# Kernel optimization log

Hardware: AMD Instinct MI355X
Metric: run time of the kernel (lower is better)

Reference implementation:

```python
import jax, jax.numpy as jnp
import numpy as np

D_MODEL = 1024
N_HEADS = 16
HEAD_DIM = D_MODEL // N_HEADS
ROPE_BASE = 10000.0


def setup_inputs() -> dict:
    key = jax.random.key(0)
    ks = jax.random.split(key, 5)
    B, S = 4, 2048
    bound_qkv = 1.0 / np.sqrt(D_MODEL)
    bound_out = 1.0 / np.sqrt(D_MODEL)
    return {
        "query": jax.random.normal(ks[0], (B, S, D_MODEL), dtype=jnp.float32),
        "W_qkv": jax.random.uniform(ks[1], (3 * D_MODEL, D_MODEL), jnp.float32, -bound_qkv, bound_qkv),
        "b_qkv": jax.random.uniform(ks[2], (3 * D_MODEL,), jnp.float32, -bound_qkv, bound_qkv),
        "W_out": jax.random.uniform(ks[3], (D_MODEL, D_MODEL), jnp.float32, -bound_out, bound_out),
        "b_out": jax.random.uniform(ks[4], (D_MODEL,), jnp.float32, -bound_out, bound_out),
    }


def _rope(x):
    # x: [B, H, S, Dh]; rotate-half RoPE, full rotational fraction
    S, Dh = x.shape[2], x.shape[3]
    half = Dh // 2
    inv_freq = 1.0 / (ROPE_BASE ** (jnp.arange(0, half, dtype=jnp.float32) * 2.0 / Dh))
    ang = jnp.arange(S, dtype=jnp.float32)[:, None] * inv_freq[None, :]  # [S, half]
    cos = jnp.concatenate([jnp.cos(ang), jnp.cos(ang)], axis=-1)  # [S, Dh]
    sin = jnp.concatenate([jnp.sin(ang), jnp.sin(ang)], axis=-1)
    x1, x2 = x[..., :half], x[..., half:]
    rot = jnp.concatenate([-x2, x1], axis=-1)
    return x * cos + rot * sin


def reference(query, W_qkv, b_qkv, W_out, b_out):
    B, S, _ = query.shape
    qkv = query @ W_qkv.T + b_qkv  # [B, S, 3*D]
    qkv = qkv.reshape(B, S, 3, N_HEADS, HEAD_DIM).transpose(2, 0, 3, 1, 4)  # [3, B, H, S, Dh]
    q, k, v = qkv[0], qkv[1], qkv[2]
    q = _rope(q)
    k = _rope(k)
    scale = 1.0 / np.sqrt(HEAD_DIM)
    scores = jnp.einsum("bhsd,bhtd->bhst", q, k) * scale  # [B, H, S, S]
    attn = jax.nn.softmax(scores, axis=-1)
    out = jnp.einsum("bhst,bhtd->bhsd", attn, v)  # [B, H, S, Dh]
    out = out.transpose(0, 2, 1, 3).reshape(B, S, D_MODEL)
    return out @ W_out.T + b_out
```

## Files before the change

### kernel.cpp

```cpp
#include <hip/hip_runtime.h>
#include <math.h>

#define D_MODEL 1024
#define N_HEADS 16
#define HEAD_DIM 64
#define BATCH 4
#define SEQ 2048
#define TOKENS (BATCH * SEQ)

typedef _Float16 f16;
typedef f16 f16x8_t __attribute__((ext_vector_type(8)));
typedef f16 f16x4_t __attribute__((ext_vector_type(4)));
typedef float f32x4_t __attribute__((ext_vector_type(4)));

#define QSCALE 0.18033688011112042f

#define KSW(row, g) ((g) ^ ((row) & 7))

__device__ __forceinline__ void stage16(const f16* g, f16* l) {
    __builtin_amdgcn_global_load_lds(
        (__attribute__((address_space(1))) void*)g,
        (__attribute__((address_space(3))) void*)l, 16, 0, 0);
}

#define N_X  (TOKENS * D_MODEL / 4)
#define N_WQ (3 * D_MODEL * D_MODEL / 4)
#define N_WO (D_MODEL * D_MODEL / 4)
#define N_CONV (N_X + N_WQ + N_WO)
__global__ void prep_kernel(const float* __restrict__ X,
                            const float* __restrict__ Wq,
                            const float* __restrict__ Wo,
                            f16* __restrict__ Xf, f16* __restrict__ Wqf,
                            f16* __restrict__ Wof,
                            float* __restrict__ cosT, float* __restrict__ sinT) {
    int i = blockIdx.x * blockDim.x + threadIdx.x;
    if (i >= N_CONV) {
        int idx = i - N_CONV;
        int s = idx >> 5;
        int ii = idx & 31;
        double t = (double)(2 * ii) / 64.0;
        double invf = pow(10000.0, -t);
        double ang = (double)s * invf;
        cosT[idx] = (float)cos(ang);
        sinT[idx] = (float)sin(ang);
        return;
    }
    const float* src;
    f16* dst;
    int j;
    if (i < N_X)             { src = X;  dst = Xf;  j = i; }
    else if (i < N_X + N_WQ) { src = Wq; dst = Wqf; j = i - N_X; }
    else                     { src = Wo; dst = Wof; j = i - N_X - N_WQ; }
    float4 x = ((const float4*)src)[j];
    f16x4_t h;
    h[0] = (f16)x.x; h[1] = (f16)x.y; h[2] = (f16)x.z; h[3] = (f16)x.w;
    ((f16x4_t*)dst)[j] = h;
}

__device__ __forceinline__ void gemm_mainloop(
    const f16* __restrict__ A, const f16* __restrict__ B,
    int n0, int c0, f16* As, f16* Bs, f32x4_t acc[4][4]) {
    const int tid = threadIdx.x;
    const int lane = tid & 63;
    const int wave = tid >> 6;
    const int m16 = lane & 15, quad = lane >> 4;
    const int wm = (wave & 1) * 64, wn = (wave >> 1) * 64;

    const int srow  = lane >> 3;
    const int sgran = (lane & 7) ^ srow;

#pragma unroll
    for (int i = 0; i < 4; i++)
#pragma unroll
        for (int j = 0; j < 4; j++) acc[i][j] = (f32x4_t){0.f, 0.f, 0.f, 0.f};

    f16* ldsA = As + (wave * 32) * 64;
    f16* ldsB = Bs + (wave * 32) * 64;
    const f16* ga = A + (size_t)(n0 + wave * 32 + srow) * D_MODEL + sgran * 8;
    const f16* gb = B + (size_t)(c0 + wave * 32 + srow) * D_MODEL + sgran * 8;

    for (int kt = 0; kt < 16; kt++) {
        const int ko = kt * 64;
        __syncthreads();
#pragma unroll
        for (int inst = 0; inst < 4; inst++) {
            stage16(ga + ko + (size_t)(inst * 8) * D_MODEL, ldsA + inst * 8 * 64);
            stage16(gb + ko + (size_t)(inst * 8) * D_MODEL, ldsB + inst * 8 * 64);
        }
        __syncthreads();
#pragma unroll
        for (int kk = 0; kk < 2; kk++) {
            f16x8_t a[4], b[4];
#pragma unroll
            for (int mt = 0; mt < 4; mt++) {
                const int row = wm + mt * 16 + m16;
                a[mt] = *(const f16x8_t*)&As[row * 64 + KSW(row, kk * 4 + quad) * 8];
            }
#pragma unroll
            for (int nt = 0; nt < 4; nt++) {
                const int row = wn + nt * 16 + m16;
                b[nt] = *(const f16x8_t*)&Bs[row * 64 + KSW(row, kk * 4 + quad) * 8];
            }
#pragma unroll
            for (int mt = 0; mt < 4; mt++)
#pragma unroll
                for (int nt = 0; nt < 4; nt++)
                    acc[mt][nt] = __builtin_amdgcn_mfma_f32_16x16x32_f16(
                        a[mt], b[nt], acc[mt][nt], 0, 0, 0);
        }
    }
}

__global__ __launch_bounds__(512)
void qkv_gemm_kernel(const f16* __restrict__ Xf, const f16* __restrict__ Wf,
                     const float* __restrict__ bias,
                     f16* __restrict__ Qb, f16* __restrict__ Kb,
                     f16* __restrict__ VbT,
                     const float* __restrict__ cosT, const float* __restrict__ sinT) {
    __shared__ f16 Ts[384 * 64];

    const int tid = threadIdx.x;
    const int lane = tid & 63;
    const int wave = tid >> 6;
    const int m16 = lane & 15, quad = lane >> 4;
    const int wm = (wave & 3) * 64, wn = (wave >> 2) * 64;

    const int n0 = blockIdx.y * 256;
    const int c0 = blockIdx.x * 128;

    const int srow8 = lane >> 3;
    const int sgran = (lane & 7) ^ srow8;

    f32x4_t acc[4][4];
#pragma unroll
    for (int i = 0; i < 4; i++)
#pragma unroll
        for (int j = 0; j < 4; j++) acc[i][j] = (f32x4_t){0.f, 0.f, 0.f, 0.f};

    const f16* ga = Xf + (size_t)(n0 + wave * 8 + srow8) * D_MODEL + sgran * 8;
    const f16* gb = Wf + (size_t)(c0 + wave * 8 + srow8) * D_MODEL + sgran * 8;
    f16* lbase = Ts + (wave * 8) * 64;

    for (int kt = 0; kt < 16; kt++) {
        const int ko = kt * 64;
        __syncthreads();
#pragma unroll
        for (int j = 0; j < 4; j++)
            stage16(ga + ko + (size_t)(j * 64) * D_MODEL, lbase + (j * 64) * 64);
#pragma unroll
        for (int j = 0; j < 2; j++)
            stage16(gb + ko + (size_t)(j * 64) * D_MODEL, lbase + ((4 + j) * 64) * 64);
        __syncthreads();
#pragma unroll
        for (int kk = 0; kk < 2; kk++) {
            f16x8_t a[4], b[4];
#pragma unroll
            for (int mt = 0; mt < 4; mt++) {
                const int row = wm + mt * 16 + m16;
                a[mt] = *(const f16x8_t*)&Ts[row * 64 + KSW(row, kk * 4 + quad) * 8];
            }
#pragma unroll
            for (int nt = 0; nt < 4; nt++) {
                const int row = 256 + wn + nt * 16 + m16;
                b[nt] = *(const f16x8_t*)&Ts[row * 64 + KSW(row, kk * 4 + quad) * 8];
            }
            __builtin_amdgcn_s_setprio(1);
#pragma unroll
            for (int mt = 0; mt < 4; mt++)
#pragma unroll
                for (int nt = 0; nt < 4; nt++)
                    acc[mt][nt] = __builtin_amdgcn_mfma_f32_16x16x32_f16(
                        a[mt], b[nt], acc[mt][nt], 0, 0, 0);
            __builtin_amdgcn_s_setprio(0);
        }
    }

    const int w = c0 >> 10;
    const int hh = ((c0 + wn) & 1023) >> 6;
    const int b = n0 >> 11;

    float bias4[4];
#pragma unroll
    for (int nt = 0; nt < 4; nt++) bias4[nt] = bias[c0 + wn + nt * 16 + m16];

    if (w == 2) {
        f16* vbase = VbT + ((size_t)(b * N_HEADS + hh) * HEAD_DIM) * SEQ;
#pragma unroll
        for (int mt = 0; mt < 4; mt++) {
            const int sbl = (n0 + wm + (mt >> 1) * 32) & (SEQ - 1);
            const int sb  = sbl + quad * 8 + (mt & 1) * 4;
#pragma unroll
            for (int nt = 0; nt < 4; nt++) {
                const int dh = nt * 16 + m16;
                f16x4_t v4;
#pragma unroll
                for (int i = 0; i < 4; i++) v4[i] = (f16)(acc[mt][nt][i] + bias4[nt]);
                *(f16x4_t*)&vbase[(size_t)dh * SEQ + sb] = v4;
            }
        }
        return;
    }

    f16* dst = (w == 0) ? Qb : Kb;
#pragma unroll
    for (int mt = 0; mt < 4; mt++)
#pragma unroll
        for (int i = 0; i < 4; i++) {
            const int n = n0 + wm + mt * 16 + quad * 4 + i;
            const int s = n & (SEQ - 1);
            f16* drow = dst + ((size_t)(b * N_HEADS + hh) * SEQ + s) * HEAD_DIM;
            float vv[4];
#pragma unroll
            for (int nt = 0; nt < 4; nt++) vv[nt] = acc[mt][nt][i] + bias4[nt];
            const float cs0 = cosT[(s << 5) + m16];
            const float sn0 = sinT[(s << 5) + m16];
            const float cs1 = cosT[(s << 5) + 16 + m16];
            const float sn1 = sinT[(s << 5) + 16 + m16];
#pragma unroll
            for (int nt = 0; nt < 4; nt++) {
                const int dh = nt * 16 + m16;
                const float cs = (nt & 1) ? cs1 : cs0;
                const float sn = (nt & 1) ? sn1 : sn0;
                const float part = vv[nt ^ 2];
                float outv = (nt >= 2) ? fmaf(vv[nt], cs, part * sn)
                                       : fmaf(vv[nt], cs, -part * sn);
                if (w == 0) outv *= QSCALE;
                drow[dh] = (f16)outv;
            }
        }
}

__global__ __launch_bounds__(256)
void out_gemm_kernel(const f16* __restrict__ Of, const f16* __restrict__ Wf,
                     const float* __restrict__ bias, float* __restrict__ Cout) {
    __shared__ f16 As[128 * 64];
    __shared__ f16 Bs[128 * 64];
    f32x4_t acc[4][4];
    const int n0 = blockIdx.y * 128;
    const int c0 = blockIdx.x * 128;
    gemm_mainloop(Of, Wf, n0, c0, As, Bs, acc);

    const int lane = threadIdx.x & 63;
    const int wave = threadIdx.x >> 6;
    const int m16 = lane & 15, quad = lane >> 4;
    const int wm = (wave & 1) * 64, wn = (wave >> 1) * 64;

    float bias4[4];
#pragma unroll
    for (int nt = 0; nt < 4; nt++) bias4[nt] = bias[c0 + wn + nt * 16 + m16];

#pragma unroll
    for (int mt = 0; mt < 4; mt++)
#pragma unroll
        for (int i = 0; i < 4; i++) {
            const int n = n0 + wm + mt * 16 + quad * 4 + i;
            float* orow = Cout + (size_t)n * D_MODEL + c0 + wn;
#pragma unroll
            for (int nt = 0; nt < 4; nt++)
                orow[nt * 16 + m16] = acc[mt][nt][i] + bias4[nt];
        }
}

#define NT (SEQ / 64)
__global__ __launch_bounds__(256, 2)
void attn_kernel(const f16* __restrict__ Qb, const f16* __restrict__ Kb,
                 const f16* __restrict__ VbT, f16* __restrict__ Of) {
    __shared__ f16 Ks[2][64 * 64];
    __shared__ f16 Vs[2][64 * 64];

    const int tid  = threadIdx.x;
    const int lane = tid & 63;
    const int wave = tid >> 6;
    const int m16  = lane & 15;
    const int quad = lane >> 4;

    const int bh = blockIdx.x & 63;
    const int qt = blockIdx.x >> 6;
    const int s0 = qt * 256;

    const f16* Kbase  = Kb + (size_t)bh * SEQ * HEAD_DIM;
    const f16* VtBase = VbT + (size_t)bh * HEAD_DIM * SEQ;

    f16x8_t bq[4][2];
#pragma unroll
    for (int nq = 0; nq < 4; nq++) {
        const f16* qrow = Qb + ((size_t)bh * SEQ + s0 + wave * 64 + nq * 16 + m16)
                          * HEAD_DIM + quad * 8;
        bq[nq][0] = *(const f16x8_t*)(qrow);
        bq[nq][1] = *(const f16x8_t*)(qrow + 32);
    }

    f32x4_t Oc[4][4];
#pragma unroll
    for (int mt = 0; mt < 4; mt++)
#pragma unroll
        for (int nq = 0; nq < 4; nq++) Oc[mt][nq] = (f32x4_t){0.f, 0.f, 0.f, 0.f};
    float sumacc[4] = {0.f, 0.f, 0.f, 0.f};

    const int lrow0 = wave * 16 + (lane >> 3);
    const int lrow1 = lrow0 + 8;
    const int gK0 = lrow0 * HEAD_DIM + KSW(lrow0, lane & 7) * 8;
    const int gK1 = lrow1 * HEAD_DIM + KSW(lrow1, lane & 7) * 8;
    const int gV0 = lrow0 * SEQ + KSW(lrow0, lane & 7) * 8;
    const int gV1 = lrow1 * SEQ + KSW(lrow1, lane & 7) * 8;
    const int lO0 = (wave * 16) * 64;
    const int lO1 = (wave * 16 + 8) * 64;

    stage16(Kbase + gK0, &Ks[0][lO0]);
    stage16(Kbase + gK1, &Ks[0][lO1]);
    stage16(VtBase + gV0, &Vs[0][lO0]);
    stage16(VtBase + gV1, &Vs[0][lO1]);
    asm volatile("s_waitcnt vmcnt(0)" ::: "memory");
    __builtin_amdgcn_s_barrier();
    asm volatile("" ::: "memory");

    for (int kt = 0; kt < NT; kt++) {
        const int cur = kt & 1;

        if (kt + 1 < NT) {
            const f16* kg = Kbase + (size_t)(kt + 1) * 64 * HEAD_DIM;
            const f16* vg = VtBase + (kt + 1) * 64;
            f16* kd = &Ks[cur ^ 1][0];
            f16* vd = &Vs[cur ^ 1][0];
            stage16(kg + gK0, kd + lO0);
            stage16(kg + gK1, kd + lO1);
            stage16(vg + gV0, vd + lO0);
            stage16(vg + gV1, vd + lO1);
        }

        const f16* Kc = &Ks[cur][0];
        const f16* Vc = &Vs[cur][0];

        f32x4_t Sc[4][4];
#pragma unroll
        for (int nt = 0; nt < 4; nt++)
#pragma unroll
            for (int nq = 0; nq < 4; nq++) Sc[nt][nq] = (f32x4_t){0.f, 0.f, 0.f, 0.f};
#pragma unroll
        for (int kki = 0; kki < 2; kki++) {
#pragma unroll
            for (int nt = 0; nt < 4; nt++) {
                const int row = nt * 16 + m16;
                f16x8_t ak = *(const f16x8_t*)&Kc[row * 64 + KSW(row, kki * 4 + quad) * 8];
                __builtin_amdgcn_s_setprio(1);
#pragma unroll
                for (int nq = 0; nq < 4; nq++)
                    Sc[nt][nq] = __builtin_amdgcn_mfma_f32_16x16x32_f16(
                        ak, bq[nq][kki], Sc[nt][nq], 0, 0, 0);
                __builtin_amdgcn_s_setprio(0);
            }
        }

#pragma unroll
        for (int kki = 0; kki < 2; kki++) {
            f16x8_t bp[4];
#pragma unroll
            for (int nq = 0; nq < 4; nq++)
#pragma unroll
                for (int h = 0; h < 2; h++) {
                    const int nt = 2 * kki + h;
#pragma unroll
                    for (int i = 0; i < 4; i++) {
                        float p = __builtin_amdgcn_exp2f(Sc[nt][nq][i]);
                        sumacc[nq] += p;
                        bp[nq][h * 4 + i] = (f16)p;
                    }
                }
#pragma unroll
            for (int mt = 0; mt < 4; mt++) {
                const int d = mt * 16 + m16;
                f16x8_t av = *(const f16x8_t*)&Vc[d * 64 + KSW(d, kki * 4 + quad) * 8];
                __builtin_amdgcn_s_setprio(1);
#pragma unroll
                for (int nq = 0; nq < 4; nq++)
                    Oc[mt][nq] = __builtin_amdgcn_mfma_f32_16x16x32_f16(
                        av, bp[nq], Oc[mt][nq], 0, 0, 0);
                __builtin_amdgcn_s_setprio(0);
            }
        }

        asm volatile("s_waitcnt vmcnt(0)" ::: "memory");
        __builtin_amdgcn_s_barrier();
        asm volatile("" ::: "memory");
    }

    const int b = bh >> 4, h = bh & 15;
#pragma unroll
    for (int nq = 0; nq < 4; nq++) {
        float l = sumacc[nq];
        l += __shfl_xor(l, 16);
        l += __shfl_xor(l, 32);
        const float invl = 1.0f / l;
        const int s = s0 + wave * 64 + nq * 16 + m16;
        const size_t off = ((size_t)(b * SEQ + s)) * D_MODEL + h * HEAD_DIM;
#pragma unroll
        for (int mt = 0; mt < 4; mt++) {
            f16x4_t o4;
#pragma unroll
            for (int i = 0; i < 4; i++)
                o4[i] = (f16)(Oc[mt][nq][i] * invl);
            *(f16x4_t*)&Of[off + mt * 16 + quad * 4] = o4;
        }
    }
}

extern "C" void kernel_launch(void* const* d_in, const int* in_sizes, int n_in,
                              void* d_out, int out_size, void* d_ws, size_t ws_size,
                              hipStream_t stream) {
    const float* X    = (const float*)d_in[0];
    const float* Wqkv = (const float*)d_in[1];
    const float* bqkv = (const float*)d_in[2];
    const float* Wout = (const float*)d_in[3];
    const float* bout = (const float*)d_in[4];
    float* out = (float*)d_out;

    char* w8 = (char*)d_ws;
    const size_t MB = 1024 * 1024;
    f16* Xf  = (f16*)(w8);
    f16* Wqf = (f16*)(w8 + 16 * MB);
    f16* Wof = (f16*)(w8 + 22 * MB);
    f16* Qf  = (f16*)(w8 + 24 * MB);
    f16* Kf  = (f16*)(w8 + 40 * MB);
    f16* VfT = (f16*)(w8 + 56 * MB);
    f16* Of  = (f16*)(w8 + 72 * MB);
    float* cosT = (float*)(w8 + 88 * MB);
    float* sinT = cosT + SEQ * 32;

    prep_kernel<<<(N_CONV + SEQ * 32) / 256, 256, 0, stream>>>(
        X, Wqkv, Wout, Xf, Wqf, Wof, cosT, sinT);

    qkv_gemm_kernel<<<dim3(3 * D_MODEL / 128, TOKENS / 256), 512, 0, stream>>>(
        Xf, Wqf, bqkv, Qf, Kf, VfT, cosT, sinT);
    attn_kernel<<<64 * (SEQ / 256), 256, 0, stream>>>(Qf, Kf, VfT, Of);
    out_gemm_kernel<<<dim3(D_MODEL / 128, TOKENS / 128), 256, 0, stream>>>(
        Of, Wof, bout, out);
}
```

Baseline: 256.6 us.

## Split attention queries across 8 waves and enlarge out-projection GEMM tile

The attention kernel now runs 512 threads per block, so each wave handles 32 query rows instead of 64. This halves the per-wave S and O accumulators to cut register pressure and raise occupancy, and each lane stages one K/V row instead of two. The output projection GEMM gets its own 256x128 tile with 8 waves, a shared LDS buffer and MFMA priority hints, replacing the shared 128x128 mainloop. The risks are more barrier overhead per K tile in attention and fewer blocks in the out GEMM.

```diff
diff --git a/kernel.cpp b/kernel.cpp
--- a/kernel.cpp
+++ b/kernel.cpp
@@ -57,60 +57,6 @@
     ((f16x4_t*)dst)[j] = h;
 }
 
-__device__ __forceinline__ void gemm_mainloop(
-    const f16* __restrict__ A, const f16* __restrict__ B,
-    int n0, int c0, f16* As, f16* Bs, f32x4_t acc[4][4]) {
-    const int tid = threadIdx.x;
-    const int lane = tid & 63;
-    const int wave = tid >> 6;
-    const int m16 = lane & 15, quad = lane >> 4;
-    const int wm = (wave & 1) * 64, wn = (wave >> 1) * 64;
-
-    const int srow  = lane >> 3;
-    const int sgran = (lane & 7) ^ srow;
-
-#pragma unroll
-    for (int i = 0; i < 4; i++)
-#pragma unroll
-        for (int j = 0; j < 4; j++) acc[i][j] = (f32x4_t){0.f, 0.f, 0.f, 0.f};
-
-    f16* ldsA = As + (wave * 32) * 64;
-    f16* ldsB = Bs + (wave * 32) * 64;
-    const f16* ga = A + (size_t)(n0 + wave * 32 + srow) * D_MODEL + sgran * 8;
-    const f16* gb = B + (size_t)(c0 + wave * 32 + srow) * D_MODEL + sgran * 8;
-
-    for (int kt = 0; kt < 16; kt++) {
-        const int ko = kt * 64;
-        __syncthreads();
-#pragma unroll
-        for (int inst = 0; inst < 4; inst++) {
-            stage16(ga + ko + (size_t)(inst * 8) * D_MODEL, ldsA + inst * 8 * 64);
-            stage16(gb + ko + (size_t)(inst * 8) * D_MODEL, ldsB + inst * 8 * 64);
-        }
-        __syncthreads();
-#pragma unroll
-        for (int kk = 0; kk < 2; kk++) {
-            f16x8_t a[4], b[4];
-#pragma unroll
-            for (int mt = 0; mt < 4; mt++) {
-                const int row = wm + mt * 16 + m16;
-                a[mt] = *(const f16x8_t*)&As[row * 64 + KSW(row, kk * 4 + quad) * 8];
-            }
-#pragma unroll
-            for (int nt = 0; nt < 4; nt++) {
-                const int row = wn + nt * 16 + m16;
-                b[nt] = *(const f16x8_t*)&Bs[row * 64 + KSW(row, kk * 4 + quad) * 8];
-            }
-#pragma unroll
-            for (int mt = 0; mt < 4; mt++)
-#pragma unroll
-                for (int nt = 0; nt < 4; nt++)
-                    acc[mt][nt] = __builtin_amdgcn_mfma_f32_16x16x32_f16(
-                        a[mt], b[nt], acc[mt][nt], 0, 0, 0);
-        }
-    }
-}
-
 __global__ __launch_bounds__(512)
 void qkv_gemm_kernel(const f16* __restrict__ Xf, const f16* __restrict__ Wf,
                      const float* __restrict__ bias,
@@ -230,20 +176,66 @@
         }
 }
 
-__global__ __launch_bounds__(256)
+__global__ __launch_bounds__(512)
 void out_gemm_kernel(const f16* __restrict__ Of, const f16* __restrict__ Wf,
                      const float* __restrict__ bias, float* __restrict__ Cout) {
-    __shared__ f16 As[128 * 64];
-    __shared__ f16 Bs[128 * 64];
+    __shared__ f16 Ts[384 * 64];
+
+    const int tid = threadIdx.x;
+    const int lane = tid & 63;
+    const int wave = tid >> 6;
+    const int m16 = lane & 15, quad = lane >> 4;
+    const int wm = (wave & 3) * 64, wn = (wave >> 2) * 64;
+
+    const int n0 = blockIdx.y * 256;
+    const int c0 = blockIdx.x * 128;
+
+    const int srow8 = lane >> 3;
+    const int sgran = (lane & 7) ^ srow8;
+
     f32x4_t acc[4][4];
-    const int n0 = blockIdx.y * 128;
-    const int c0 = blockIdx.x * 128;
-    gemm_mainloop(Of, Wf, n0, c0, As, Bs, acc);
-
-    const int lane = threadIdx.x & 63;
-    const int wave = threadIdx.x >> 6;
-    const int m16 = lane & 15, quad = lane >> 4;
-    const int wm = (wave & 1) * 64, wn = (wave >> 1) * 64;
+#pragma unroll
+    for (int i = 0; i < 4; i++)
+#pragma unroll
+        for (int j = 0; j < 4; j++) acc[i][j] = (f32x4_t){0.f, 0.f, 0.f, 0.f};
+
+    const f16* ga = Of + (size_t)(n0 + wave * 8 + srow8) * D_MODEL + sgran * 8;
+    const f16* gb = Wf + (size_t)(c0 + wave * 8 + srow8) * D_MODEL + sgran * 8;
+    f16* lbase = Ts + (wave * 8) * 64;
+
+    for (int kt = 0; kt < 16; kt++) {
+        const int ko = kt * 64;
+        __syncthreads();
+#pragma unroll
+        for (int j = 0; j < 4; j++)
+            stage16(ga + ko + (size_t)(j * 64) * D_MODEL, lbase + (j * 64) * 64);
+#pragma unroll
+        for (int j = 0; j < 2; j++)
+            stage16(gb + ko + (size_t)(j * 64) * D_MODEL, lbase + ((4 + j) * 64) * 64);
+        __syncthreads();
+#pragma unroll
+        for (int kk = 0; kk < 2; kk++) {
+            f16x8_t a[4], b[4];
+#pragma unroll
+            for (int mt = 0; mt < 4; mt++) {
+                const int row = wm + mt * 16 + m16;
+                a[mt] = *(const f16x8_t*)&Ts[row * 64 + KSW(row, kk * 4 + quad) * 8];
+            }
+#pragma unroll
+            for (int nt = 0; nt < 4; nt++) {
+                const int row = 256 + wn + nt * 16 + m16;
+                b[nt] = *(const f16x8_t*)&Ts[row * 64 + KSW(row, kk * 4 + quad) * 8];
+            }
+            __builtin_amdgcn_s_setprio(1);
+#pragma unroll
+            for (int mt = 0; mt < 4; mt++)
+#pragma unroll
+                for (int nt = 0; nt < 4; nt++)
+                    acc[mt][nt] = __builtin_amdgcn_mfma_f32_16x16x32_f16(
+                        a[mt], b[nt], acc[mt][nt], 0, 0, 0);
+            __builtin_amdgcn_s_setprio(0);
+        }
+    }
 
     float bias4[4];
 #pragma unroll
@@ -262,7 +254,7 @@
 }
 
 #define NT (SEQ / 64)
-__global__ __launch_bounds__(256, 2)
+__global__ __launch_bounds__(512, 4)
 void attn_kernel(const f16* __restrict__ Qb, const f16* __restrict__ Kb,
                  const f16* __restrict__ VbT, f16* __restrict__ Of) {
     __shared__ f16 Ks[2][64 * 64];
@@ -281,35 +273,29 @@
     const f16* Kbase  = Kb + (size_t)bh * SEQ * HEAD_DIM;
     const f16* VtBase = VbT + (size_t)bh * HEAD_DIM * SEQ;
 
-    f16x8_t bq[4][2];
-#pragma unroll
-    for (int nq = 0; nq < 4; nq++) {
-        const f16* qrow = Qb + ((size_t)bh * SEQ + s0 + wave * 64 + nq * 16 + m16)
+    f16x8_t bq[2][2];
+#pragma unroll
+    for (int nq = 0; nq < 2; nq++) {
+        const f16* qrow = Qb + ((size_t)bh * SEQ + s0 + wave * 32 + nq * 16 + m16)
                           * HEAD_DIM + quad * 8;
         bq[nq][0] = *(const f16x8_t*)(qrow);
         bq[nq][1] = *(const f16x8_t*)(qrow + 32);
     }
 
-    f32x4_t Oc[4][4];
+    f32x4_t Oc[4][2];
 #pragma unroll
     for (int mt = 0; mt < 4; mt++)
 #pragma unroll
-        for (int nq = 0; nq < 4; nq++) Oc[mt][nq] = (f32x4_t){0.f, 0.f, 0.f, 0.f};
-    float sumacc[4] = {0.f, 0.f, 0.f, 0.f};
-
-    const int lrow0 = wave * 16 + (lane >> 3);
-    const int lrow1 = lrow0 + 8;
-    const int gK0 = lrow0 * HEAD_DIM + KSW(lrow0, lane & 7) * 8;
-    const int gK1 = lrow1 * HEAD_DIM + KSW(lrow1, lane & 7) * 8;
-    const int gV0 = lrow0 * SEQ + KSW(lrow0, lane & 7) * 8;
-    const int gV1 = lrow1 * SEQ + KSW(lrow1, lane & 7) * 8;
-    const int lO0 = (wave * 16) * 64;
-    const int lO1 = (wave * 16 + 8) * 64;
-
-    stage16(Kbase + gK0, &Ks[0][lO0]);
-    stage16(Kbase + gK1, &Ks[0][lO1]);
-    stage16(VtBase + gV0, &Vs[0][lO0]);
-    stage16(VtBase + gV1, &Vs[0][lO1]);
+        for (int nq = 0; nq < 2; nq++) Oc[mt][nq] = (f32x4_t){0.f, 0.f, 0.f, 0.f};
+    float sumacc[2] = {0.f, 0.f};
+
+    const int lrow = wave * 8 + (lane >> 3);
+    const int gK = lrow * HEAD_DIM + KSW(lrow, lane & 7) * 8;
+    const int gV = lrow * SEQ + KSW(lrow, lane & 7) * 8;
+    const int lO = (wave * 8) * 64;
+
+    stage16(Kbase + gK, &Ks[0][lO]);
+    stage16(VtBase + gV, &Vs[0][lO]);
     asm volatile("s_waitcnt vmcnt(0)" ::: "memory");
     __builtin_amdgcn_s_barrier();
     asm volatile("" ::: "memory");
@@ -320,22 +306,18 @@
         if (kt + 1 < NT) {
             const f16* kg = Kbase + (size_t)(kt + 1) * 64 * HEAD_DIM;
             const f16* vg = VtBase + (kt + 1) * 64;
-            f16* kd = &Ks[cur ^ 1][0];
-            f16* vd = &Vs[cur ^ 1][0];
-            stage16(kg + gK0, kd + lO0);
-            stage16(kg + gK1, kd + lO1);
-            stage16(vg + gV0, vd + lO0);
-            stage16(vg + gV1, vd + lO1);
+            stage16(kg + gK, &Ks[cur ^ 1][lO]);
+            stage16(vg + gV, &Vs[cur ^ 1][lO]);
         }
 
         const f16* Kc = &Ks[cur][0];
         const f16* Vc = &Vs[cur][0];
 
-        f32x4_t Sc[4][4];
+        f32x4_t Sc[4][2];
 #pragma unroll
         for (int nt = 0; nt < 4; nt++)
 #pragma unroll
-            for (int nq = 0; nq < 4; nq++) Sc[nt][nq] = (f32x4_t){0.f, 0.f, 0.f, 0.f};
+            for (int nq = 0; nq < 2; nq++) Sc[nt][nq] = (f32x4_t){0.f, 0.f, 0.f, 0.f};
 #pragma unroll
         for (int kki = 0; kki < 2; kki++) {
 #pragma unroll
@@ -344,7 +326,7 @@
                 f16x8_t ak = *(const f16x8_t*)&Kc[row * 64 + KSW(row, kki * 4 + quad) * 8];
                 __builtin_amdgcn_s_setprio(1);
 #pragma unroll
-                for (int nq = 0; nq < 4; nq++)
+                for (int nq = 0; nq < 2; nq++)
                     Sc[nt][nq] = __builtin_amdgcn_mfma_f32_16x16x32_f16(
                         ak, bq[nq][kki], Sc[nt][nq], 0, 0, 0);
                 __builtin_amdgcn_s_setprio(0);
@@ -353,9 +335,9 @@
 
 #pragma unroll
         for (int kki = 0; kki < 2; kki++) {
-            f16x8_t bp[4];
-#pragma unroll
-            for (int nq = 0; nq < 4; nq++)
+            f16x8_t bp[2];
+#pragma unroll
+            for (int nq = 0; nq < 2; nq++)
 #pragma unroll
                 for (int h = 0; h < 2; h++) {
                     const int nt = 2 * kki + h;
@@ -372,7 +354,7 @@
                 f16x8_t av = *(const f16x8_t*)&Vc[d * 64 + KSW(d, kki * 4 + quad) * 8];
                 __builtin_amdgcn_s_setprio(1);
 #pragma unroll
-                for (int nq = 0; nq < 4; nq++)
+                for (int nq = 0; nq < 2; nq++)
                     Oc[mt][nq] = __builtin_amdgcn_mfma_f32_16x16x32_f16(
                         av, bp[nq], Oc[mt][nq], 0, 0, 0);
                 __builtin_amdgcn_s_setprio(0);
@@ -386,12 +368,12 @@
 
     const int b = bh >> 4, h = bh & 15;
 #pragma unroll
-    for (int nq = 0; nq < 4; nq++) {
+    for (int nq = 0; nq < 2; nq++) {
         float l = sumacc[nq];
         l += __shfl_xor(l, 16);
         l += __shfl_xor(l, 32);
         const float invl = 1.0f / l;
-        const int s = s0 + wave * 64 + nq * 16 + m16;
+        const int s = s0 + wave * 32 + nq * 16 + m16;
         const size_t off = ((size_t)(b * SEQ + s)) * D_MODEL + h * HEAD_DIM;
 #pragma unroll
         for (int mt = 0; mt < 4; mt++) {
@@ -431,7 +413,7 @@
 
     qkv_gemm_kernel<<<dim3(3 * D_MODEL / 128, TOKENS / 256), 512, 0, stream>>>(
         Xf, Wqf, bqkv, Qf, Kf, VfT, cosT, sinT);
-    attn_kernel<<<64 * (SEQ / 256), 256, 0, stream>>>(Qf, Kf, VfT, Of);
-    out_gemm_kernel<<<dim3(D_MODEL / 128, TOKENS / 128), 256, 0, stream>>>(
+    attn_kernel<<<64 * (SEQ / 256), 512, 0, stream>>>(Qf, Kf, VfT, Of);
+    out_gemm_kernel<<<dim3(D_MODEL / 128, TOKENS / 256), 512, 0, stream>>>(
         Of, Wof, bout, out);
 }
```

Result: slower. 273.0 us (+6.4%).

## Double-buffer QKV GEMM LDS staging with smaller 128x128 tiles

Applied to the files above, without the earlier changes.

The QKV projection GEMM moves from a 256x128 tile with 512 threads and a single LDS buffer to a 128x128 tile with 256 threads and double-buffered A/B tiles in LDS. The next K-slice is prefetched through global_load_lds while the current slice feeds the MFMAs, leaving one barrier per iteration instead of two. The goal is to hide global load latency and allow two blocks per CU. The trade-off is twice as many blocks and more total global traffic, because each W tile is now re-read by twice as many row blocks.

```diff
diff --git a/kernel.cpp b/kernel.cpp
--- a/kernel.cpp
+++ b/kernel.cpp
@@ -111,25 +111,26 @@
     }
 }
 
-__global__ __launch_bounds__(512)
+__global__ __launch_bounds__(256, 2)
 void qkv_gemm_kernel(const f16* __restrict__ Xf, const f16* __restrict__ Wf,
                      const float* __restrict__ bias,
                      f16* __restrict__ Qb, f16* __restrict__ Kb,
                      f16* __restrict__ VbT,
                      const float* __restrict__ cosT, const float* __restrict__ sinT) {
-    __shared__ f16 Ts[384 * 64];
+    __shared__ f16 As[2][128 * 64];
+    __shared__ f16 Bs[2][128 * 64];
 
     const int tid = threadIdx.x;
     const int lane = tid & 63;
     const int wave = tid >> 6;
     const int m16 = lane & 15, quad = lane >> 4;
-    const int wm = (wave & 3) * 64, wn = (wave >> 2) * 64;
-
-    const int n0 = blockIdx.y * 256;
+    const int wm = (wave & 1) * 64, wn = (wave >> 1) * 64;
+
+    const int n0 = blockIdx.y * 128;
     const int c0 = blockIdx.x * 128;
 
-    const int srow8 = lane >> 3;
-    const int sgran = (lane & 7) ^ srow8;
+    const int srow  = lane >> 3;
+    const int sgran = (lane & 7) ^ srow;
 
     f32x4_t acc[4][4];
 #pragma unroll
@@ -137,32 +138,47 @@
 #pragma unroll
         for (int j = 0; j < 4; j++) acc[i][j] = (f32x4_t){0.f, 0.f, 0.f, 0.f};
 
-    const f16* ga = Xf + (size_t)(n0 + wave * 8 + srow8) * D_MODEL + sgran * 8;
-    const f16* gb = Wf + (size_t)(c0 + wave * 8 + srow8) * D_MODEL + sgran * 8;
-    f16* lbase = Ts + (wave * 8) * 64;
+    const f16* ga = Xf + (size_t)(n0 + wave * 32 + srow) * D_MODEL + sgran * 8;
+    const f16* gb = Wf + (size_t)(c0 + wave * 32 + srow) * D_MODEL + sgran * 8;
+    const int lO = (wave * 32) * 64;
+
+#pragma unroll
+    for (int inst = 0; inst < 4; inst++) {
+        stage16(ga + (size_t)(inst * 8) * D_MODEL, &As[0][lO + inst * 8 * 64]);
+        stage16(gb + (size_t)(inst * 8) * D_MODEL, &Bs[0][lO + inst * 8 * 64]);
+    }
+    asm volatile("s_waitcnt vmcnt(0)" ::: "memory");
+    __builtin_amdgcn_s_barrier();
+    asm volatile("" ::: "memory");
 
     for (int kt = 0; kt < 16; kt++) {
-        const int ko = kt * 64;
-        __syncthreads();
-#pragma unroll
-        for (int j = 0; j < 4; j++)
-            stage16(ga + ko + (size_t)(j * 64) * D_MODEL, lbase + (j * 64) * 64);
-#pragma unroll
-        for (int j = 0; j < 2; j++)
-            stage16(gb + ko + (size_t)(j * 64) * D_MODEL, lbase + ((4 + j) * 64) * 64);
-        __syncthreads();
+        const int cur = kt & 1;
+
+        if (kt + 1 < 16) {
+            const int ko = (kt + 1) * 64;
+#pragma unroll
+            for (int inst = 0; inst < 4; inst++) {
+                stage16(ga + ko + (size_t)(inst * 8) * D_MODEL,
+                        &As[cur ^ 1][lO + inst * 8 * 64]);
+                stage16(gb + ko + (size_t)(inst * 8) * D_MODEL,
+                        &Bs[cur ^ 1][lO + inst * 8 * 64]);
+            }
+        }
+
+        const f16* Ac = &As[cur][0];
+        const f16* Bc = &Bs[cur][0];
 #pragma unroll
         for (int kk = 0; kk < 2; kk++) {
             f16x8_t a[4], b[4];
 #pragma unroll
             for (int mt = 0; mt < 4; mt++) {
                 const int row = wm + mt * 16 + m16;
-                a[mt] = *(const f16x8_t*)&Ts[row * 64 + KSW(row, kk * 4 + quad) * 8];
+                a[mt] = *(const f16x8_t*)&Ac[row * 64 + KSW(row, kk * 4 + quad) * 8];
             }
 #pragma unroll
             for (int nt = 0; nt < 4; nt++) {
-                const int row = 256 + wn + nt * 16 + m16;
-                b[nt] = *(const f16x8_t*)&Ts[row * 64 + KSW(row, kk * 4 + quad) * 8];
+                const int row = wn + nt * 16 + m16;
+                b[nt] = *(const f16x8_t*)&Bc[row * 64 + KSW(row, kk * 4 + quad) * 8];
             }
             __builtin_amdgcn_s_setprio(1);
 #pragma unroll
@@ -173,6 +189,10 @@
                         a[mt], b[nt], acc[mt][nt], 0, 0, 0);
             __builtin_amdgcn_s_setprio(0);
         }
+
+        asm volatile("s_waitcnt vmcnt(0)" ::: "memory");
+        __builtin_amdgcn_s_barrier();
+        asm volatile("" ::: "memory");
     }
 
     const int w = c0 >> 10;
@@ -429,7 +449,7 @@
     prep_kernel<<<(N_CONV + SEQ * 32) / 256, 256, 0, stream>>>(
         X, Wqkv, Wout, Xf, Wqf, Wof, cosT, sinT);
 
-    qkv_gemm_kernel<<<dim3(3 * D_MODEL / 128, TOKENS / 256), 512, 0, stream>>>(
+    qkv_gemm_kernel<<<dim3(3 * D_MODEL / 128, TOKENS / 128), 256, 0, stream>>>(
         Xf, Wqf, bqkv, Qf, Kf, VfT, cosT, sinT);
     attn_kernel<<<64 * (SEQ / 256), 256, 0, stream>>>(Qf, Kf, VfT, Of);
     out_gemm_kernel<<<dim3(D_MODEL / 128, TOKENS / 128), 256, 0, stream>>>(
```

After: 256.6 us. No clear change (-0.0%).
